# Kernel tuning notes

Hardware: AMD Instinct MI355X
Metric: run time of the kernel (lower is better)

Reference implementation:

```python
import jax, jax.numpy as jnp
import numpy as np

N_NODES = 65536
N_EDGES = 1048576
D_FEAT = 64
UNITS = 64


def setup_inputs() -> dict:
    key = jax.random.key(0)
    k1, k2, k3, k4, k5 = jax.random.split(key, 5)
    nodes = jax.random.normal(k1, (N_NODES, D_FEAT), dtype=jnp.float32)
    edge_vals = jax.random.uniform(k2, (N_EDGES,), dtype=jnp.float32)
    kernel = jax.random.normal(k3, (D_FEAT, UNITS), dtype=jnp.float32) * (1.0 / np.sqrt(D_FEAT))
    src_idx = jax.random.randint(k4, (N_EDGES,), 0, N_NODES, dtype=jnp.int32)
    dst_idx = jnp.sort(jax.random.randint(k5, (N_EDGES,), 0, N_NODES, dtype=jnp.int32))
    return {"nodes": nodes, "edge_vals": edge_vals, "kernel": kernel,
            "src_idx": src_idx, "dst_idx": dst_idx}


def reference(nodes, edge_vals, kernel, src_idx, dst_idx):
    # sparse_dense_matmul(A, X): for each edge (dst, src, w): agg[dst] += w * X[src]
    msgs = edge_vals[:, None] * nodes[src_idx]          # [E, d]
    agg = jax.ops.segment_sum(msgs, dst_idx, num_segments=nodes.shape[0])  # [N, d]
    # dense projection (activation is None -> linear)
    return agg @ kernel                                  # [N, units]
```

## Files before the change

### kernel.cpp

```cpp
#include <hip/hip_runtime.h>
#include <hip/hip_bf16.h>


constexpr int D = 64;
constexpr int EPW = 128;

__global__ __launch_bounds__(256) void zero_kernel(float4* __restrict__ p, int n4) {
    int i = blockIdx.x * blockDim.x + threadIdx.x;
    int stride = gridDim.x * blockDim.x;
    for (; i < n4; i += stride) p[i] = make_float4(0.f, 0.f, 0.f, 0.f);
}

__global__ __launch_bounds__(256) void gemm_nodes_bf16(const float* __restrict__ nodes,
                                                       const float* __restrict__ Km,
                                                       __hip_bfloat16* __restrict__ P,
                                                       int n_nodes) {
    __shared__ float Ks[D * D];
    const int t = threadIdx.x;
    for (int i = t; i < D * D / 4; i += 256)
        ((float4*)Ks)[i] = ((const float4*)Km)[i];
    __syncthreads();

    const int rx = t & 31, uy = t >> 5;
    const long R0 = (long)blockIdx.x * 128 + rx * 4;
    const int u0 = uy * 8;

    float acc[4][8];
    #pragma unroll
    for (int i = 0; i < 4; ++i)
        #pragma unroll
        for (int j = 0; j < 8; ++j) acc[i][j] = 0.f;

    #pragma unroll 4
    for (int dq = 0; dq < 16; ++dq) {
        float a_s[4][4];
        #pragma unroll
        for (int i = 0; i < 4; ++i) {
            long row = R0 + i; if (row >= n_nodes) row = n_nodes - 1;
            const float4 g = *(const float4*)&nodes[row * D + dq * 4];
            a_s[i][0] = g.x; a_s[i][1] = g.y; a_s[i][2] = g.z; a_s[i][3] = g.w;
        }
        #pragma unroll
        for (int di = 0; di < 4; ++di) {
            const float4 k0 = *(const float4*)&Ks[(dq * 4 + di) * D + u0];
            const float4 k1 = *(const float4*)&Ks[(dq * 4 + di) * D + u0 + 4];
            const float kv[8] = {k0.x, k0.y, k0.z, k0.w, k1.x, k1.y, k1.z, k1.w};
            #pragma unroll
            for (int i = 0; i < 4; ++i)
                #pragma unroll
                for (int j = 0; j < 8; ++j)
                    acc[i][j] = fmaf(a_s[i][di], kv[j], acc[i][j]);
        }
    }

    #pragma unroll
    for (int i = 0; i < 4; ++i) {
        long row = R0 + i;
        if (row < n_nodes) {
            ushort u[8];
            #pragma unroll
            for (int j = 0; j < 8; ++j) {
                __hip_bfloat16 b = __float2bfloat16(acc[i][j]);
                u[j] = *(ushort*)&b;
            }
            uint4 pk;
            pk.x = (uint)u[0] | ((uint)u[1] << 16);
            pk.y = (uint)u[2] | ((uint)u[3] << 16);
            pk.z = (uint)u[4] | ((uint)u[5] << 16);
            pk.w = (uint)u[6] | ((uint)u[7] << 16);
            *(uint4*)&P[row * D + u0] = pk;
        }
    }
}

template <typename T>
__device__ __forceinline__ float load_feat(const T* P, long idx);
template <>
__device__ __forceinline__ float load_feat<__hip_bfloat16>(const __hip_bfloat16* P, long idx) {
    return __bfloat162float(P[idx]);
}
template <>
__device__ __forceinline__ float load_feat<float>(const float* P, long idx) { return P[idx]; }

template <typename T>
__global__ __launch_bounds__(256) void scatter_sorted(
    const T* __restrict__ P, const float* __restrict__ evals,
    const int* __restrict__ src, const int* __restrict__ dst,
    float* __restrict__ out, int n_edges)
{
    const int lane = threadIdx.x & 63;
    const int wid  = blockIdx.x * (blockDim.x >> 6) + (threadIdx.x >> 6);
    const long base = (long)wid * EPW;
    if (base >= n_edges) return;

    const int first = dst[base];
    int prev = first;
    float acc = 0.f;

    if (base + EPW <= n_edges) {
        #pragma unroll 1
        for (int i0 = 0; i0 < EPW; i0 += 16) {
            const int4*   sp = (const int4*)  &src[base + i0];
            const int4*   dp = (const int4*)  &dst[base + i0];
            const float4* wp = (const float4*)&evals[base + i0];
            const int4   sv0 = sp[0], sv1 = sp[1], sv2 = sp[2], sv3 = sp[3];
            const int4   dv0 = dp[0], dv1 = dp[1], dv2 = dp[2], dv3 = dp[3];
            const float4 wv0 = wp[0], wv1 = wp[1], wv2 = wp[2], wv3 = wp[3];

            const int svs[16] = {sv0.x, sv0.y, sv0.z, sv0.w, sv1.x, sv1.y, sv1.z, sv1.w,
                                 sv2.x, sv2.y, sv2.z, sv2.w, sv3.x, sv3.y, sv3.z, sv3.w};
            float v[16];
            #pragma unroll
            for (int k = 0; k < 16; ++k) v[k] = load_feat<T>(P, (long)svs[k] * D + lane);

            const int   dvs[16] = {dv0.x, dv0.y, dv0.z, dv0.w, dv1.x, dv1.y, dv1.z, dv1.w,
                                   dv2.x, dv2.y, dv2.z, dv2.w, dv3.x, dv3.y, dv3.z, dv3.w};
            const float wvs[16] = {wv0.x, wv0.y, wv0.z, wv0.w, wv1.x, wv1.y, wv1.z, wv1.w,
                                   wv2.x, wv2.y, wv2.z, wv2.w, wv3.x, wv3.y, wv3.z, wv3.w};
            #pragma unroll
            for (int k = 0; k < 16; ++k) {
                if (dvs[k] != prev) {
                    float* o = &out[(long)prev * D + lane];
                    if (prev == first) atomicAdd(o, acc);
                    else               *o = acc;
                    acc = 0.f;
                    prev = dvs[k];
                }
                acc = fmaf(wvs[k], v[k], acc);
            }
        }
    } else {
        for (long e = base; e < n_edges; ++e) {
            int s = src[e], dc = dst[e]; float w = evals[e];
            float v = load_feat<T>(P, (long)s * D + lane);
            if (dc != prev) {
                float* o = &out[(long)prev * D + lane];
                if (prev == first) atomicAdd(o, acc);
                else               *o = acc;
                acc = 0.f;
                prev = dc;
            }
            acc = fmaf(w, v, acc);
        }
    }
    atomicAdd(&out[(long)prev * D + lane], acc);
}

__global__ __launch_bounds__(256) void project_inplace(float* __restrict__ out,
                                                       const float* __restrict__ Km, int n_nodes) {
    __shared__ float Ks[D * D];
    const int t = threadIdx.x;
    for (int i = t; i < D * D; i += 256) Ks[i] = Km[i];
    __syncthreads();
    const int lane = t & 63;
    const int n = blockIdx.x * 4 + (t >> 6);
    if (n >= n_nodes) return;
    float* row = out + (long)n * D;
    const float rv = row[lane];
    float acc = 0.f;
    #pragma unroll
    for (int d = 0; d < D; ++d) acc = fmaf(__shfl(rv, d), Ks[d * D + lane], acc);
    row[lane] = acc;
}

extern "C" void kernel_launch(void* const* d_in, const int* in_sizes, int n_in,
                              void* d_out, int out_size, void* d_ws, size_t ws_size,
                              hipStream_t stream) {
    const float* nodes = (const float*)d_in[0];
    const float* evals = (const float*)d_in[1];
    const float* Km    = (const float*)d_in[2];
    const int*   src   = (const int*)d_in[3];
    const int*   dst   = (const int*)d_in[4];
    float* out = (float*)d_out;

    const int n_nodes = in_sizes[0] / D;
    const int n_edges = in_sizes[1];
    const int n_waves = (n_edges + EPW - 1) / EPW;

    zero_kernel<<<2048, 256, 0, stream>>>((float4*)out, out_size / 4);

    const size_t need = (size_t)n_nodes * D * sizeof(__hip_bfloat16);
    if (ws_size >= need) {
        __hip_bfloat16* P = (__hip_bfloat16*)d_ws;
        gemm_nodes_bf16<<<(n_nodes + 127) / 128, 256, 0, stream>>>(nodes, Km, P, n_nodes);
        scatter_sorted<__hip_bfloat16><<<(n_waves + 3) / 4, 256, 0, stream>>>(
            P, evals, src, dst, out, n_edges);
    } else {
        scatter_sorted<float><<<(n_waves + 3) / 4, 256, 0, stream>>>(
            nodes, evals, src, dst, out, n_edges);
        project_inplace<<<(n_nodes + 3) / 4, 256, 0, stream>>>(out, Km, n_nodes);
    }
}
```

Before: 131.3 us.

## Rewrite node GEMM as wave-per-row with register-held weights; uniformize scatter base

The node projection GEMM now keeps one column of the weight matrix in registers per lane. Each wave walks 8 rows, loading each row with wave-uniform (scalar-friendly) float4 loads and doing a 64-term dot product per lane. This replaces the shared-memory tiled 4x8 register-blocked GEMM and writes one bf16 per lane instead of packed 8-wide stores. In the scatter kernel the edge base offset is made wave-uniform via readfirstlane, so the index, dst and weight loads can use scalar addressing. The trade is much more register pressure (64 weight registers plus a 64-float row), narrower output stores and fewer FMAs per loaded value.

```diff
diff --git a/kernel.cpp b/kernel.cpp
--- a/kernel.cpp
+++ b/kernel.cpp
@@ -11,65 +11,38 @@
     for (; i < n4; i += stride) p[i] = make_float4(0.f, 0.f, 0.f, 0.f);
 }
 
-__global__ __launch_bounds__(256) void gemm_nodes_bf16(const float* __restrict__ nodes,
-                                                       const float* __restrict__ Km,
-                                                       __hip_bfloat16* __restrict__ P,
-                                                       int n_nodes) {
-    __shared__ float Ks[D * D];
-    const int t = threadIdx.x;
-    for (int i = t; i < D * D / 4; i += 256)
-        ((float4*)Ks)[i] = ((const float4*)Km)[i];
-    __syncthreads();
+__global__ __launch_bounds__(256) void gemm_rows(const float* __restrict__ nodes,
+                                                 const float* __restrict__ Km,
+                                                 __hip_bfloat16* __restrict__ P,
+                                                 int n_nodes) {
+    const int lane = threadIdx.x & 63;
+    float kcol[D];
+    #pragma unroll
+    for (int d = 0; d < D; ++d) kcol[d] = Km[d * D + lane];
 
-    const int rx = t & 31, uy = t >> 5;
-    const long R0 = (long)blockIdx.x * 128 + rx * 4;
-    const int u0 = uy * 8;
+    const int wid = (blockIdx.x * blockDim.x + threadIdx.x) >> 6;
+    const int urow0 = __builtin_amdgcn_readfirstlane(wid * 8);
 
-    float acc[4][8];
-    #pragma unroll
-    for (int i = 0; i < 4; ++i)
+    #pragma unroll 1
+    for (int i = 0; i < 8; ++i) {
+        const int row = urow0 + i;
+        if (row >= n_nodes) return;
+        const float4* rp = (const float4*)(nodes + (long)row * D);
+        float4 a[16];
         #pragma unroll
-        for (int j = 0; j < 8; ++j) acc[i][j] = 0.f;
-
-    #pragma unroll 4
-    for (int dq = 0; dq < 16; ++dq) {
-        float a_s[4][4];
+        for (int q = 0; q < 16; ++q) a[q] = rp[q];
+        const float* af = (const float*)a;
+        float acc0 = 0.f, acc1 = 0.f, acc2 = 0.f, acc3 = 0.f;
         #pragma unroll
-        for (int i = 0; i < 4; ++i) {
-            long row = R0 + i; if (row >= n_nodes) row = n_nodes - 1;
-            const float4 g = *(const float4*)&nodes[row * D + dq * 4];
-            a_s[i][0] = g.x; a_s[i][1] = g.y; a_s[i][2] = g.z; a_s[i][3] = g.w;
+        for (int d = 0; d < D; d += 4) {
+            acc0 = fmaf(af[d + 0], kcol[d + 0], acc0);
+            acc1 = fmaf(af[d + 1], kcol[d + 1], acc1);
+            acc2 = fmaf(af[d + 2], kcol[d + 2], acc2);
+            acc3 = fmaf(af[d + 3], kcol[d + 3], acc3);
         }
-        #pragma unroll
-        for (int di = 0; di < 4; ++di) {
-            const float4 k0 = *(const float4*)&Ks[(dq * 4 + di) * D + u0];
-            const float4 k1 = *(const float4*)&Ks[(dq * 4 + di) * D + u0 + 4];
-            const float kv[8] = {k0.x, k0.y, k0.z, k0.w, k1.x, k1.y, k1.z, k1.w};
-            #pragma unroll
-            for (int i = 0; i < 4; ++i)
-                #pragma unroll
-                for (int j = 0; j < 8; ++j)
-                    acc[i][j] = fmaf(a_s[i][di], kv[j], acc[i][j]);
-        }
-    }
-
-    #pragma unroll
-    for (int i = 0; i < 4; ++i) {
-        long row = R0 + i;
-        if (row < n_nodes) {
-            ushort u[8];
-            #pragma unroll
-            for (int j = 0; j < 8; ++j) {
-                __hip_bfloat16 b = __float2bfloat16(acc[i][j]);
-                u[j] = *(ushort*)&b;
-            }
-            uint4 pk;
-            pk.x = (uint)u[0] | ((uint)u[1] << 16);
-            pk.y = (uint)u[2] | ((uint)u[3] << 16);
-            pk.z = (uint)u[4] | ((uint)u[5] << 16);
-            pk.w = (uint)u[6] | ((uint)u[7] << 16);
-            *(uint4*)&P[row * D + u0] = pk;
-        }
+        const float acc = (acc0 + acc1) + (acc2 + acc3);
+        __hip_bfloat16 b = __float2bfloat16(acc);
+        P[(long)row * D + lane] = b;
     }
 }
 
@@ -92,17 +65,18 @@
     const int wid  = blockIdx.x * (blockDim.x >> 6) + (threadIdx.x >> 6);
     const long base = (long)wid * EPW;
     if (base >= n_edges) return;
+    const int ubase = __builtin_amdgcn_readfirstlane((int)base);
 
-    const int first = dst[base];
+    const int first = dst[ubase];
     int prev = first;
     float acc = 0.f;
 
-    if (base + EPW <= n_edges) {
+    if ((long)ubase + EPW <= (long)n_edges) {
         #pragma unroll 1
         for (int i0 = 0; i0 < EPW; i0 += 16) {
-            const int4*   sp = (const int4*)  &src[base + i0];
-            const int4*   dp = (const int4*)  &dst[base + i0];
-            const float4* wp = (const float4*)&evals[base + i0];
+            const int4*   sp = (const int4*)  (src   + ubase + i0);
+            const int4*   dp = (const int4*)  (dst   + ubase + i0);
+            const float4* wp = (const float4*)(evals + ubase + i0);
             const int4   sv0 = sp[0], sv1 = sp[1], sv2 = sp[2], sv3 = sp[3];
             const int4   dv0 = dp[0], dv1 = dp[1], dv2 = dp[2], dv3 = dp[3];
             const float4 wv0 = wp[0], wv1 = wp[1], wv2 = wp[2], wv3 = wp[3];
@@ -111,7 +85,10 @@
                                  sv2.x, sv2.y, sv2.z, sv2.w, sv3.x, sv3.y, sv3.z, sv3.w};
             float v[16];
             #pragma unroll
-            for (int k = 0; k < 16; ++k) v[k] = load_feat<T>(P, (long)svs[k] * D + lane);
+            for (int k = 0; k < 16; ++k) {
+                const T* prow = P + (long)svs[k] * D;
+                v[k] = load_feat<T>(prow, lane);
+            }
 
             const int   dvs[16] = {dv0.x, dv0.y, dv0.z, dv0.w, dv1.x, dv1.y, dv1.z, dv1.w,
                                    dv2.x, dv2.y, dv2.z, dv2.w, dv3.x, dv3.y, dv3.z, dv3.w};
@@ -130,7 +107,7 @@
             }
         }
     } else {
-        for (long e = base; e < n_edges; ++e) {
+        for (long e = ubase; e < n_edges; ++e) {
             int s = src[e], dc = dst[e]; float w = evals[e];
             float v = load_feat<T>(P, (long)s * D + lane);
             if (dc != prev) {
@@ -182,7 +159,8 @@
     const size_t need = (size_t)n_nodes * D * sizeof(__hip_bfloat16);
     if (ws_size >= need) {
         __hip_bfloat16* P = (__hip_bfloat16*)d_ws;
-        gemm_nodes_bf16<<<(n_nodes + 127) / 128, 256, 0, stream>>>(nodes, Km, P, n_nodes);
+        const int gw = (n_nodes + 7) / 8;
+        gemm_rows<<<(gw + 3) / 4, 256, 0, stream>>>(nodes, Km, P, n_nodes);
         scatter_sorted<__hip_bfloat16><<<(n_waves + 3) / 4, 256, 0, stream>>>(
             P, evals, src, dst, out, n_edges);
     } else {
```

Result: faster. 116.6 us (-11.2%).
